# Optimization experiments

Measured on AMD Instinct MI355X. Metric: run time of the kernel, lower is better.

Reference implementation:

```python
import jax, jax.numpy as jnp
import numpy as np
from jax import lax

E, O, I, K = 8, 256, 128, 3  # num_experts, out_ch, in_ch, kernel
HID = 32  # routing hidden dim


def setup_inputs() -> dict:
    key = jax.random.key(0)
    ks = jax.random.split(key, 7)
    B, H, W = 32, 56, 56
    x = jax.random.normal(ks[0], (B, I, H, W), dtype=jnp.float32)
    # kaiming_normal fan_out for (E,O,I,K,K): fan_out = O*K*K
    std = float(np.sqrt(2.0 / (O * K * K)))
    weight = jax.random.normal(ks[1], (E, O, I, K, K), dtype=jnp.float32) * std
    bias = jax.random.normal(ks[2], (E, O), dtype=jnp.float32)
    # routing MLP: Linear(I,32) -> ReLU -> Linear(32,E) -> softmax
    w1 = jax.random.normal(ks[3], (HID, I), dtype=jnp.float32) / np.sqrt(I)
    b1 = jax.random.normal(ks[4], (HID,), dtype=jnp.float32) * 0.01
    w2 = jax.random.normal(ks[5], (E, HID), dtype=jnp.float32) / np.sqrt(HID)
    b2 = jax.random.normal(ks[6], (E,), dtype=jnp.float32) * 0.01
    return {"x": x, "weight": weight, "bias": bias, "w1": w1, "b1": b1, "w2": w2, "b2": b2}


def reference(x, weight, bias, w1, b1, w2, b2):
    # routing: global avg pool -> MLP -> softmax over experts
    pooled = x.mean(axis=(2, 3))                      # (B, I)
    h = jax.nn.relu(pooled @ w1.T + b1)               # (B, 32)
    r = jax.nn.softmax(h @ w2.T + b2, axis=1)         # (B, E)
    # per-sample combined kernel and bias
    cw = jnp.einsum('be,eoihw->boihw', r, weight)     # (B, O, I, K, K)
    cb = r @ bias                                     # (B, O)
    # per-sample conv (equivalent to groups=batch trick), stride=1, padding=1
    def conv_one(xi, wi):
        return lax.conv_general_dilated(
            xi[None], wi, window_strides=(1, 1), padding=[(1, 1), (1, 1)],
            dimension_numbers=('NCHW', 'OIHW', 'NCHW'))[0]
    out = jax.vmap(conv_one)(x, cw)                   # (B, O, H, W)
    return out + cb[:, :, None, None]
```

## Files before the change

### kernel.cpp

```cpp
#include <hip/hip_runtime.h>

#define E_ 8
#define O_ 256
#define I_ 128
#define B_ 32
#define H_ 56
#define W_ 56
#define HP 58
#define HW (H_*W_)
#define KK 9

typedef __attribute__((ext_vector_type(8))) short short8;
typedef __attribute__((ext_vector_type(4))) float float4_;

#define XP_ELEMS (B_*HP*HP*I_)
#define POOL_OFF ((size_t)XP_ELEMS*2)
#define R_OFF    (POOL_OFF + (size_t)B_*I_*4)
#define CWT_OFF  (R_OFF + (size_t)B_*E_*4)

__device__ __forceinline__ unsigned short f2bf(float f) {
  union { float f; unsigned u; } v; v.f = f;
  unsigned r = v.u + 0x7FFFu + ((v.u >> 16) & 1u);
  return (unsigned short)(r >> 16);
}

__device__ __forceinline__ void gload16(const unsigned short* g, unsigned short* l) {
  __builtin_amdgcn_global_load_lds(
      (const __attribute__((address_space(1))) unsigned int*)g,
      (__attribute__((address_space(3))) unsigned int*)l, 16, 0, 0);
}

__global__ void k1_pool_pack(const float* __restrict__ x,
                             unsigned short* __restrict__ xp,
                             float* __restrict__ pooled) {
  __shared__ float lds[I_*57];
  const int h = blockIdx.x, b = blockIdx.y, tid = threadIdx.x;
  const float* xb = x + (size_t)b*I_*HW + h*W_;
  for (int idx = tid; idx < I_*W_; idx += 256) {
    int ic = idx / W_, wv = idx - ic*W_;
    lds[ic*57 + wv] = xb[(size_t)ic*HW + wv];
  }
  __syncthreads();
  if (tid < I_) {
    float s = 0.f;
    #pragma unroll 8
    for (int wv = 0; wv < W_; ++wv) s += lds[tid*57 + wv];
    atomicAdd(&pooled[b*I_ + tid], s);
  }
  unsigned short* xrow = xp + ((size_t)(b*HP + h + 1)*HP)*I_;
  for (int idx2 = tid; idx2 < W_*(I_/2); idx2 += 256) {
    int wv = idx2 >> 6, ic2 = idx2 & 63;
    unsigned short u0 = f2bf(lds[(ic2*2)*57 + wv]);
    unsigned short u1 = f2bf(lds[(ic2*2+1)*57 + wv]);
    *(unsigned*)&xrow[(wv+1)*I_ + ic2*2] = (unsigned)u0 | ((unsigned)u1 << 16);
  }
  if (tid < I_) {
    xrow[0*I_ + tid] = 0;
    xrow[57*I_ + tid] = 0;
  }
  if (h == 0) {
    unsigned short* r0 = xp + (size_t)(b*HP)*HP*I_;
    for (int idx = tid; idx < HP*I_; idx += 256) r0[idx] = 0;
  }
  if (h == H_-1) {
    unsigned short* r57 = xp + (size_t)((b*HP + 57)*HP)*I_;
    for (int idx = tid; idx < HP*I_; idx += 256) r57[idx] = 0;
  }
}

__global__ void k2_route(const float* __restrict__ pooled,
                         const float* __restrict__ w1, const float* __restrict__ b1,
                         const float* __restrict__ w2, const float* __restrict__ b2,
                         float* __restrict__ r) {
  __shared__ float p[I_];
  __shared__ float hh[32];
  __shared__ float lg[8];
  const int b = blockIdx.x, tid = threadIdx.x;
  if (tid < 64) {
    p[tid]      = pooled[b*I_ + tid]      * (1.f/HW);
    p[tid + 64] = pooled[b*I_ + tid + 64] * (1.f/HW);
  }
  __syncthreads();
  if (tid < 32) {
    float s = b1[tid];
    for (int i = 0; i < I_; ++i) s += p[i]*w1[tid*I_ + i];
    hh[tid] = s > 0.f ? s : 0.f;
  }
  __syncthreads();
  if (tid < 8) {
    float s = b2[tid];
    for (int j = 0; j < 32; ++j) s += hh[j]*w2[tid*32 + j];
    lg[tid] = s;
  }
  __syncthreads();
  if (tid == 0) {
    float m = lg[0];
    for (int e = 1; e < 8; ++e) m = fmaxf(m, lg[e]);
    float ex[8], sum = 0.f;
    for (int e = 0; e < 8; ++e) { ex[e] = expf(lg[e]-m); sum += ex[e]; }
    float inv = 1.f/sum;
    for (int e = 0; e < 8; ++e) r[b*8 + e] = ex[e]*inv;
  }
}

__global__ void k3_combine(const float* __restrict__ weight, const float* __restrict__ r,
                           unsigned short* __restrict__ cwT) {
  __shared__ float wl[E_*1152];
  const int o = blockIdx.x, tid = threadIdx.x;
  for (int e = 0; e < E_; ++e)
    for (int idx = tid; idx < 1152; idx += 256)
      wl[e*1152 + idx] = weight[(size_t)(e*O_ + o)*1152 + idx];
  __syncthreads();
  for (int b = 0; b < B_; ++b) {
    float rb[E_];
    #pragma unroll
    for (int e = 0; e < E_; ++e) rb[e] = r[b*E_ + e];
    for (int idx2 = tid; idx2 < 576; idx2 += 256) {
      int t = idx2 >> 6, ic2 = idx2 & 63;
      int ic = ic2*2;
      float v0 = 0.f, v1 = 0.f;
      #pragma unroll
      for (int e = 0; e < E_; ++e) {
        v0 += rb[e]*wl[e*1152 + ic*9 + t];
        v1 += rb[e]*wl[e*1152 + (ic+1)*9 + t];
      }
      *(unsigned*)&cwT[((size_t)(b*KK + t)*O_ + o)*I_ + ic] =
          (unsigned)f2bf(v0) | ((unsigned)f2bf(v1) << 16);
    }
  }
}

__global__ __launch_bounds__(256)
void k4_conv(const unsigned short* __restrict__ xp,
             const unsigned short* __restrict__ cwT,
             const float* __restrict__ r, const float* __restrict__ bias,
             float* __restrict__ out) {
  __shared__ __align__(16) unsigned short ldsA[128*64];
  __shared__ __align__(16) unsigned short ldsB[128*64];
  __shared__ float cbs[128];

  const int tid  = threadIdx.x;
  const int lane = tid & 63;
  const int wave = tid >> 6;
  const int n0 = blockIdx.x * 128;
  const int m0 = blockIdx.y * 128;
  const int b  = blockIdx.z;

  if (tid < 128) {
    float s = 0.f;
    #pragma unroll
    for (int e = 0; e < 8; ++e) s += r[b*8 + e]*bias[e*O_ + m0 + tid];
    cbs[tid] = s;
  }

  const int q = lane >> 4, l16 = lane & 15;
  const int lrow = lane >> 3, lchk = lane & 7;
  const int chunk = lchk ^ lrow;
  const int wm0 = (wave >> 1) * 64;
  const int wn0 = (wave & 1) * 64;

  int ainv[4], binv[4];
  #pragma unroll
  for (int j = 0; j < 4; ++j) {
    int row = wave*32 + j*8 + lrow;
    ainv[j] = row*I_ + chunk*8;
    int p = n0 + (wave + 4*j)*8 + lrow;
    int pc = p < HW ? p : HW-1;
    int rj = pc / 56, wj = pc - rj*56;
    binv[j] = ((b*HP + rj)*HP + wj)*I_ + chunk*8;
  }
  int xq[2], rowA[4], rowB[4];
  #pragma unroll
  for (int s = 0; s < 2; ++s) xq[s] = ((s*4 + q) ^ (l16 & 7))*8;
  #pragma unroll
  for (int f = 0; f < 4; ++f) rowA[f] = (wm0 + f*16 + l16)*64;
  #pragma unroll
  for (int g = 0; g < 4; ++g) rowB[g] = (wn0 + g*16 + l16)*64;

  float4_ acc[4][4];
  #pragma unroll
  for (int f = 0; f < 4; ++f)
    #pragma unroll
    for (int g = 0; g < 4; ++g) acc[f][g] = (float4_){0.f, 0.f, 0.f, 0.f};

  for (int kh = 0; kh < 3; ++kh)
  for (int kw = 0; kw < 3; ++kw) {
    const int tap = kh*3 + kw;
    #pragma unroll
    for (int icc = 0; icc < 2; ++icc) {
      __syncthreads();
      const unsigned short* abase = cwT + (((size_t)(b*KK + tap)*O_ + m0)*I_ + icc*64);
      #pragma unroll
      for (int j = 0; j < 4; ++j)
        gload16(abase + ainv[j], &ldsA[(wave*32 + j*8)*64]);
      const unsigned short* bbase = xp + ((kh*HP + kw)*I_ + icc*64);
      #pragma unroll
      for (int j = 0; j < 4; ++j)
        gload16(bbase + binv[j], &ldsB[((wave + 4*j)*8)*64]);
      __syncthreads();
      #pragma unroll
      for (int s = 0; s < 2; ++s) {
        short8 af[4], bfr[4];
        #pragma unroll
        for (int f = 0; f < 4; ++f) af[f] = *(const short8*)&ldsA[rowA[f] + xq[s]];
        #pragma unroll
        for (int g = 0; g < 4; ++g) bfr[g] = *(const short8*)&ldsB[rowB[g] + xq[s]];
        #pragma unroll
        for (int f = 0; f < 4; ++f)
          #pragma unroll
          for (int g = 0; g < 4; ++g)
            acc[f][g] = __builtin_amdgcn_mfma_f32_16x16x32_bf16(af[f], bfr[g], acc[f][g], 0, 0, 0);
      }
    }
  }

  #pragma unroll
  for (int g = 0; g < 4; ++g) {
    int p = n0 + wn0 + g*16 + l16;
    if (p < HW) {
      #pragma unroll
      for (int f = 0; f < 4; ++f) {
        #pragma unroll
        for (int v = 0; v < 4; ++v) {
          int ml = wm0 + f*16 + q*4 + v;
          out[(size_t)(b*O_ + m0 + ml)*HW + p] = acc[f][g][v] + cbs[ml];
        }
      }
    }
  }
}

extern "C" void kernel_launch(void* const* d_in, const int* in_sizes, int n_in,
                              void* d_out, int out_size, void* d_ws, size_t ws_size,
                              hipStream_t stream) {
  const float* x      = (const float*)d_in[0];
  const float* weight = (const float*)d_in[1];
  const float* bias   = (const float*)d_in[2];
  const float* w1     = (const float*)d_in[3];
  const float* b1     = (const float*)d_in[4];
  const float* w2     = (const float*)d_in[5];
  const float* b2     = (const float*)d_in[6];
  float* out = (float*)d_out;
  char* ws = (char*)d_ws;

  unsigned short* xp     = (unsigned short*)(ws);
  float*          pooled = (float*)(ws + POOL_OFF);
  float*          rr     = (float*)(ws + R_OFF);
  unsigned short* cwT    = (unsigned short*)(ws + CWT_OFF);

  hipMemsetAsync(pooled, 0, B_*I_*sizeof(float), stream);
  k1_pool_pack<<<dim3(H_, B_), 256, 0, stream>>>(x, xp, pooled);
  k2_route<<<B_, 64, 0, stream>>>(pooled, w1, b1, w2, b2, rr);
  k3_combine<<<O_, 256, 0, stream>>>(weight, rr, cwT);
  k4_conv<<<dim3(25, 2, B_), 256, 0, stream>>>(xp, cwT, rr, bias, out);
}
```

Baseline: 280.6 us.

## Load padded input patch once per tile and reuse across all nine conv taps

The conv kernel now tiles by 4 output rows (224 pixels) and stages a padded 6x58 input patch in LDS once per channel chunk. All nine taps read shifted views of that patch instead of reloading the B tile per tap, and the weight tile is double-buffered so the next tap's load overlaps the current MFMAs. Pooling uses per-row partial sums reduced in the routing kernel instead of atomics plus a memset, and the combine kernel splits the batch over two blocks. Per-thread accumulators and LDS use grow, which may reduce occupancy despite the 2-block launch bound.

New measurement: 258.4 us. 1.09x faster.

```diff
diff --git a/kernel.cpp b/kernel.cpp
--- a/kernel.cpp
+++ b/kernel.cpp
@@ -10,12 +10,16 @@
 #define HW (H_*W_)
 #define KK 9
 
+#define NROW 4
+#define NPIX 224
+#define PPIX 348
+
 typedef __attribute__((ext_vector_type(8))) short short8;
 typedef __attribute__((ext_vector_type(4))) float float4_;
 
 #define XP_ELEMS (B_*HP*HP*I_)
 #define POOL_OFF ((size_t)XP_ELEMS*2)
-#define R_OFF    (POOL_OFF + (size_t)B_*I_*4)
+#define R_OFF    (POOL_OFF + (size_t)B_*H_*I_*4)
 #define CWT_OFF  (R_OFF + (size_t)B_*E_*4)
 
 __device__ __forceinline__ unsigned short f2bf(float f) {
@@ -32,7 +36,7 @@
 
 __global__ void k1_pool_pack(const float* __restrict__ x,
                              unsigned short* __restrict__ xp,
-                             float* __restrict__ pooled) {
+                             float* __restrict__ pooled_part) {
   __shared__ float lds[I_*57];
   const int h = blockIdx.x, b = blockIdx.y, tid = threadIdx.x;
   const float* xb = x + (size_t)b*I_*HW + h*W_;
@@ -45,7 +49,7 @@
     float s = 0.f;
     #pragma unroll 8
     for (int wv = 0; wv < W_; ++wv) s += lds[tid*57 + wv];
-    atomicAdd(&pooled[b*I_ + tid], s);
+    pooled_part[(size_t)(b*H_ + h)*I_ + tid] = s;
   }
   unsigned short* xrow = xp + ((size_t)(b*HP + h + 1)*HP)*I_;
   for (int idx2 = tid; idx2 < W_*(I_/2); idx2 += 256) {
@@ -68,7 +72,7 @@
   }
 }
 
-__global__ void k2_route(const float* __restrict__ pooled,
+__global__ void k2_route(const float* __restrict__ pooled_part,
                          const float* __restrict__ w1, const float* __restrict__ b1,
                          const float* __restrict__ w2, const float* __restrict__ b2,
                          float* __restrict__ r) {
@@ -76,9 +80,10 @@
   __shared__ float hh[32];
   __shared__ float lg[8];
   const int b = blockIdx.x, tid = threadIdx.x;
-  if (tid < 64) {
-    p[tid]      = pooled[b*I_ + tid]      * (1.f/HW);
-    p[tid + 64] = pooled[b*I_ + tid + 64] * (1.f/HW);
+  if (tid < I_) {
+    float s = 0.f;
+    for (int h = 0; h < H_; ++h) s += pooled_part[(size_t)(b*H_ + h)*I_ + tid];
+    p[tid] = s * (1.f/HW);
   }
   __syncthreads();
   if (tid < 32) {
@@ -107,11 +112,12 @@
                            unsigned short* __restrict__ cwT) {
   __shared__ float wl[E_*1152];
   const int o = blockIdx.x, tid = threadIdx.x;
+  const int b0 = blockIdx.y * 16;
   for (int e = 0; e < E_; ++e)
     for (int idx = tid; idx < 1152; idx += 256)
       wl[e*1152 + idx] = weight[(size_t)(e*O_ + o)*1152 + idx];
   __syncthreads();
-  for (int b = 0; b < B_; ++b) {
+  for (int b = b0; b < b0 + 16; ++b) {
     float rb[E_];
     #pragma unroll
     for (int e = 0; e < E_; ++e) rb[e] = r[b*E_ + e];
@@ -130,21 +136,21 @@
   }
 }
 
-__global__ __launch_bounds__(256)
+__global__ __launch_bounds__(256, 2)
 void k4_conv(const unsigned short* __restrict__ xp,
              const unsigned short* __restrict__ cwT,
              const float* __restrict__ r, const float* __restrict__ bias,
              float* __restrict__ out) {
-  __shared__ __align__(16) unsigned short ldsA[128*64];
-  __shared__ __align__(16) unsigned short ldsB[128*64];
+  __shared__ __align__(16) unsigned short patch[PPIX*64];
+  __shared__ __align__(16) unsigned short ldsA[2][128*64];
   __shared__ float cbs[128];
 
   const int tid  = threadIdx.x;
   const int lane = tid & 63;
   const int wave = tid >> 6;
-  const int n0 = blockIdx.x * 128;
-  const int m0 = blockIdx.y * 128;
-  const int b  = blockIdx.z;
+  const int gr0 = blockIdx.x * NROW;
+  const int m0  = blockIdx.y * 128;
+  const int b   = blockIdx.z;
 
   if (tid < 128) {
     float s = 0.f;
@@ -154,77 +160,92 @@
   }
 
   const int q = lane >> 4, l16 = lane & 15;
-  const int lrow = lane >> 3, lchk = lane & 7;
-  const int chunk = lchk ^ lrow;
+  const int lrow = lane >> 3, chunk = (lane & 7) ^ lrow;
   const int wm0 = (wave >> 1) * 64;
-  const int wn0 = (wave & 1) * 64;
-
-  int ainv[4], binv[4];
-  #pragma unroll
-  for (int j = 0; j < 4; ++j) {
-    int row = wave*32 + j*8 + lrow;
-    ainv[j] = row*I_ + chunk*8;
-    int p = n0 + (wave + 4*j)*8 + lrow;
-    int pc = p < HW ? p : HW-1;
-    int rj = pc / 56, wj = pc - rj*56;
-    binv[j] = ((b*HP + rj)*HP + wj)*I_ + chunk*8;
-  }
-  int xq[2], rowA[4], rowB[4];
+  const int wn0 = (wave & 1) * 112;
+
+  int ainv[4];
+  #pragma unroll
+  for (int j = 0; j < 4; ++j)
+    ainv[j] = (wave*32 + j*8 + lrow)*I_ + chunk*8;
+  int rowA[4];
+  #pragma unroll
+  for (int f = 0; f < 4; ++f) rowA[f] = (wm0 + f*16 + l16)*64;
+  int xq[2];
   #pragma unroll
   for (int s = 0; s < 2; ++s) xq[s] = ((s*4 + q) ^ (l16 & 7))*8;
-  #pragma unroll
-  for (int f = 0; f < 4; ++f) rowA[f] = (wm0 + f*16 + l16)*64;
-  #pragma unroll
-  for (int g = 0; g < 4; ++g) rowB[g] = (wn0 + g*16 + l16)*64;
-
-  float4_ acc[4][4];
+  int bg[7];
+  #pragma unroll
+  for (int g = 0; g < 7; ++g) {
+    int p = wn0 + g*16 + l16;
+    int rr_ = p / 56;
+    bg[g] = rr_*58 + (p - rr_*56);
+  }
+
+  float4_ acc[4][7];
   #pragma unroll
   for (int f = 0; f < 4; ++f)
     #pragma unroll
-    for (int g = 0; g < 4; ++g) acc[f][g] = (float4_){0.f, 0.f, 0.f, 0.f};
-
-  for (int kh = 0; kh < 3; ++kh)
-  for (int kw = 0; kw < 3; ++kw) {
-    const int tap = kh*3 + kw;
-    #pragma unroll
-    for (int icc = 0; icc < 2; ++icc) {
+    for (int g = 0; g < 7; ++g) acc[f][g] = (float4_){0.f, 0.f, 0.f, 0.f};
+
+  const unsigned short* xpb = xp + (size_t)((b*HP + gr0)*HP)*I_;
+
+  for (int icc = 0; icc < 2; ++icc) {
+    __syncthreads();
+    for (int it = 0; it < 11; ++it) {
+      int c = it*256 + tid;
+      if (c < PPIX*8) {
+        int pp = c >> 3, k8 = c & 7;
+        short8 v = *(const short8*)(xpb + (size_t)pp*I_ + icc*64 + k8*8);
+        *(short8*)&patch[pp*64 + ((k8 ^ (pp & 7))*8)] = v;
+      }
+    }
+    {
+      const unsigned short* ab = cwT + ((size_t)(b*KK)*O_ + m0)*I_ + icc*64;
+      #pragma unroll
+      for (int j = 0; j < 4; ++j)
+        gload16(ab + ainv[j], &ldsA[0][(wave*32 + j*8)*64]);
+    }
+    for (int tap = 0; tap < 9; ++tap) {
       __syncthreads();
-      const unsigned short* abase = cwT + (((size_t)(b*KK + tap)*O_ + m0)*I_ + icc*64);
-      #pragma unroll
-      for (int j = 0; j < 4; ++j)
-        gload16(abase + ainv[j], &ldsA[(wave*32 + j*8)*64]);
-      const unsigned short* bbase = xp + ((kh*HP + kw)*I_ + icc*64);
-      #pragma unroll
-      for (int j = 0; j < 4; ++j)
-        gload16(bbase + binv[j], &ldsB[((wave + 4*j)*8)*64]);
-      __syncthreads();
+      if (tap < 8) {
+        const unsigned short* ab = cwT + ((size_t)(b*KK + tap + 1)*O_ + m0)*I_ + icc*64;
+        #pragma unroll
+        for (int j = 0; j < 4; ++j)
+          gload16(ab + ainv[j], &ldsA[(tap + 1) & 1][(wave*32 + j*8)*64]);
+      }
+      const unsigned short* At = ldsA[tap & 1];
+      const int kh = tap / 3, kw = tap - kh*3;
+      const int toff = kh*58 + kw;
       #pragma unroll
       for (int s = 0; s < 2; ++s) {
-        short8 af[4], bfr[4];
-        #pragma unroll
-        for (int f = 0; f < 4; ++f) af[f] = *(const short8*)&ldsA[rowA[f] + xq[s]];
-        #pragma unroll
-        for (int g = 0; g < 4; ++g) bfr[g] = *(const short8*)&ldsB[rowB[g] + xq[s]];
+        short8 af[4], bfr[7];
+        #pragma unroll
+        for (int f = 0; f < 4; ++f) af[f] = *(const short8*)&At[rowA[f] + xq[s]];
+        #pragma unroll
+        for (int g = 0; g < 7; ++g) {
+          int pp = bg[g] + toff;
+          bfr[g] = *(const short8*)&patch[pp*64 + (((s*4 + q) ^ (pp & 7))*8)];
+        }
         #pragma unroll
         for (int f = 0; f < 4; ++f)
           #pragma unroll
-          for (int g = 0; g < 4; ++g)
+          for (int g = 0; g < 7; ++g)
             acc[f][g] = __builtin_amdgcn_mfma_f32_16x16x32_bf16(af[f], bfr[g], acc[f][g], 0, 0, 0);
       }
     }
   }
 
-  #pragma unroll
-  for (int g = 0; g < 4; ++g) {
-    int p = n0 + wn0 + g*16 + l16;
-    if (p < HW) {
-      #pragma unroll
-      for (int f = 0; f < 4; ++f) {
-        #pragma unroll
-        for (int v = 0; v < 4; ++v) {
-          int ml = wm0 + f*16 + q*4 + v;
-          out[(size_t)(b*O_ + m0 + ml)*HW + p] = acc[f][g][v] + cbs[ml];
-        }
+  const size_t obase = (size_t)(b*O_ + m0)*HW + gr0*W_;
+  #pragma unroll
+  for (int g = 0; g < 7; ++g) {
+    int p = wn0 + g*16 + l16;
+    #pragma unroll
+    for (int f = 0; f < 4; ++f) {
+      #pragma unroll
+      for (int v = 0; v < 4; ++v) {
+        int ml = wm0 + f*16 + q*4 + v;
+        out[obase + (size_t)ml*HW + p] = acc[f][g][v] + cbs[ml];
       }
     }
   }
@@ -244,13 +265,12 @@
   char* ws = (char*)d_ws;
 
   unsigned short* xp     = (unsigned short*)(ws);
-  float*          pooled = (float*)(ws + POOL_OFF);
+  float*          ppart  = (float*)(ws + POOL_OFF);
   float*          rr     = (float*)(ws + R_OFF);
   unsigned short* cwT    = (unsigned short*)(ws + CWT_OFF);
 
-  hipMemsetAsync(pooled, 0, B_*I_*sizeof(float), stream);
-  k1_pool_pack<<<dim3(H_, B_), 256, 0, stream>>>(x, xp, pooled);
-  k2_route<<<B_, 64, 0, stream>>>(pooled, w1, b1, w2, b2, rr);
-  k3_combine<<<O_, 256, 0, stream>>>(weight, rr, cwT);
-  k4_conv<<<dim3(25, 2, B_), 256, 0, stream>>>(xp, cwT, rr, bias, out);
-}
+  k1_pool_pack<<<dim3(H_, B_), 256, 0, stream>>>(x, xp, ppart);
+  k2_route<<<B_, 128, 0, stream>>>(ppart, w1, b1, w2, b2, rr);
+  k3_combine<<<dim3(O_, 2), 256, 0, stream>>>(weight, rr, cwT);
+  k4_conv<<<dim3(H_/NROW, 2, B_), 256, 0, stream>>>(xp, cwT, rr, bias, out);
+}
```
